# Kernel tuning notes

Measured on AMD Instinct MI355X. Metric: run time of the kernel, lower is better.

The kernel has to match this reference:

```python
import jax, jax.numpy as jnp
import numpy as np

EMBED_DIM = 1024
NUM_HEADS = 16
HEAD_DIM = EMBED_DIM // NUM_HEADS
B, S = 4, 2048


def setup_inputs() -> dict:
    key = jax.random.key(0)
    ks = jax.random.split(key, 9)
    scale = 1.0 / np.sqrt(EMBED_DIM)
    inp = {
        "inputs": jax.random.normal(ks[0], (B, S, EMBED_DIM), dtype=jnp.float32),
        "rotation_params": jax.random.normal(ks[1], (B, S, EMBED_DIM), dtype=jnp.float32),
        "entangle_params": jax.random.normal(ks[2], (B, S, EMBED_DIM), dtype=jnp.float32),
        # Linear weights stored as (out, in) like torch; applied as x @ W.T
        "Wq": jax.random.normal(ks[3], (EMBED_DIM, EMBED_DIM), dtype=jnp.float32) * scale,
        "Wk": jax.random.normal(ks[4], (EMBED_DIM, EMBED_DIM), dtype=jnp.float32) * scale,
        "Wv": jax.random.normal(ks[5], (EMBED_DIM, EMBED_DIM), dtype=jnp.float32) * scale,
        "Wrot": jax.random.normal(ks[6], (EMBED_DIM, EMBED_DIM), dtype=jnp.float32) * scale,
        "Went": jax.random.normal(ks[7], (EMBED_DIM, EMBED_DIM), dtype=jnp.float32) * scale,
        "Wo": jax.random.normal(ks[8], (EMBED_DIM, EMBED_DIM), dtype=jnp.float32) * scale,
    }
    return inp


def _split_heads(x):
    b, s, e = x.shape
    return x.reshape(b, s, NUM_HEADS, HEAD_DIM).transpose(0, 2, 1, 3)  # (B,H,S,D)


def reference(inputs, rotation_params, entangle_params, Wq, Wk, Wv, Wrot, Went, Wo):
    Q = inputs @ Wq.T + rotation_params @ Wrot.T
    K = inputs @ Wk.T + entangle_params @ Went.T
    V = inputs @ Wv.T
    Qh, Kh, Vh = _split_heads(Q), _split_heads(K), _split_heads(V)
    scores = jnp.einsum("bhqd,bhkd->bhqk", Qh, Kh) / jnp.sqrt(jnp.float32(HEAD_DIM))
    attn = jax.nn.softmax(scores, axis=-1)  # dropout p=0 -> identity
    out = jnp.einsum("bhqk,bhkd->bhqd", attn, Vh)
    out = out.transpose(0, 2, 1, 3).reshape(inputs.shape[0], inputs.shape[1], EMBED_DIM)
    return out @ Wo.T
```

## Files before the change

### kernel.cpp

```cpp
#include <hip/hip_runtime.h>
#include <stdint.h>


typedef unsigned short u16;
typedef __bf16 bf16x8 __attribute__((ext_vector_type(8)));
typedef float f32x4 __attribute__((ext_vector_type(4)));
typedef float f32x16 __attribute__((ext_vector_type(16)));
typedef uint32_t u32x4 __attribute__((ext_vector_type(4)));

#define MFMA_BF16(a, b, c) __builtin_amdgcn_mfma_f32_16x16x32_bf16((a), (b), (c), 0, 0, 0)
#define MFMA32(a, b, c)    __builtin_amdgcn_mfma_f32_32x32x16_bf16((a), (b), (c), 0, 0, 0)
#define GAMMA 0.18033688011112042f
#define BHSTRIDE 131072

static __device__ __forceinline__ u16 f2bf(float f) {
    uint32_t u = __builtin_bit_cast(uint32_t, f);
    u = (u + 0x7FFFu + ((u >> 16) & 1u)) >> 16;
    return (u16)u;
}

static __device__ __forceinline__ uint32_t pk_rne2(float a, float b) {
    uint32_t ua = __builtin_bit_cast(uint32_t, a);
    uint32_t ub = __builtin_bit_cast(uint32_t, b);
    ua += 0x7FFFu + ((ua >> 16) & 1u);
    ub += 0x7FFFu + ((ub >> 16) & 1u);
    return __builtin_amdgcn_perm(ub, ua, 0x07060302);
}

static __device__ __forceinline__ void async_copy16(const void* g, void* l) {
    __builtin_amdgcn_global_load_lds((__attribute__((address_space(1))) void*)g,
                                     (__attribute__((address_space(3))) void*)l,
                                     16, 0, 0);
}

static __device__ __forceinline__ uint32_t cvtpk(float a, float b) {
    uint32_t r;
    asm("v_cvt_pk_bf16_f32 %0, %1, %2" : "=v"(r) : "v"(a), "v"(b));
    return r;
}

static __device__ __forceinline__ void plswap(uint32_t& a, uint32_t& b) {
    asm("v_permlane32_swap_b32 %0, %1" : "+v"(a), "+v"(b));
}

static __device__ __forceinline__ bf16x8 mkfrag(uint32_t w0, uint32_t w1,
                                                uint32_t w2, uint32_t w3) {
    u32x4 u = {w0, w1, w2, w3};
    return __builtin_bit_cast(bf16x8, u);
}

struct CvtArgs { const float* s[6]; u16* d[6]; };

__global__ __launch_bounds__(256) void cvt_kernel(CvtArgs a, int nelem) {
    const float* s = a.s[blockIdx.z];
    u16* d = a.d[blockIdx.z];
    int i = (blockIdx.x * 256 + threadIdx.x) * 8;
    float4 f0 = *(const float4*)(s + i);
    float4 f1 = *(const float4*)(s + i + 4);
    uint4 w;
    w.x = pk_rne2(f0.x, f0.y); w.y = pk_rne2(f0.z, f0.w);
    w.z = pk_rne2(f1.x, f1.y); w.w = pk_rne2(f1.z, f1.w);
    *(uint4*)(d + i) = w;
}

template <int AMODE, int CMODE>
__global__ __launch_bounds__(256, 2) void gemm_bt(
    const u16* __restrict__ A0, const u16* __restrict__ W0,
    const u16* __restrict__ A1, const u16* __restrict__ W1,
    void* __restrict__ Cv, int K, int npairs, float scale)
{
    __shared__ __align__(16) u16 lA[128 * 64];
    __shared__ __align__(16) u16 lB[128 * 64];

    const int tid  = threadIdx.x;
    const int lane = tid & 63;
    const int wave = tid >> 6;
    const int wm   = (wave >> 1) * 64;
    const int wn   = (wave & 1) * 64;
    const size_t m0 = (size_t)blockIdx.x * 128;
    const size_t n0 = (size_t)blockIdx.y * 128;

    const int row8 = tid >> 3;
    const int cp   = tid & 7;
    const int fr   = lane & 15;
    const int g    = lane >> 4;

    const size_t bb = (m0 >> 11) * 16;
    const size_t s0 = m0 & 2047;

    f32x4 acc[4][4] = {};

    for (int p = 0; p < npairs; ++p) {
        const u16* A = p ? A1 : A0;
        const u16* W = p ? W1 : W0;
        for (int k0 = 0; k0 < K; k0 += 64) {
            __syncthreads();
#pragma unroll
            for (int it = 0; it < 4; ++it) {
                int row = it * 32 + row8;
                int sc = cp ^ (((row >> 3) ^ row) & 7);
                if (AMODE == 0) {
                    async_copy16(A + ((m0 + row) * (size_t)K + k0 + sc * 8),
                                 (char*)lA + it * 4096 + tid * 16);
                } else {
                    size_t base = (bb + (size_t)(k0 >> 6)) * BHSTRIDE;
                    async_copy16(A + base + (s0 + row) * 64 + sc * 8,
                                 (char*)lA + it * 4096 + tid * 16);
                }
                async_copy16(W + ((n0 + row) * (size_t)K + k0 + sc * 8),
                             (char*)lB + it * 4096 + tid * 16);
            }
            __syncthreads();

            bf16x8 af[4][2], bfm[4][2];
#pragma unroll
            for (int i = 0; i < 4; ++i) {
                int row = wm + i * 16 + fr;
                int sw = ((row >> 3) ^ row) & 7;
                af[i][0] = *(const bf16x8*)(lA + row * 64 + (g ^ sw) * 8);
                af[i][1] = *(const bf16x8*)(lA + row * 64 + ((4 + g) ^ sw) * 8);
            }
#pragma unroll
            for (int j = 0; j < 4; ++j) {
                int row = wn + j * 16 + fr;
                int sw = ((row >> 3) ^ row) & 7;
                bfm[j][0] = *(const bf16x8*)(lB + row * 64 + (g ^ sw) * 8);
                bfm[j][1] = *(const bf16x8*)(lB + row * 64 + ((4 + g) ^ sw) * 8);
            }
#pragma unroll
            for (int i = 0; i < 4; ++i)
#pragma unroll
                for (int j = 0; j < 4; ++j) {
                    acc[i][j] = MFMA_BF16(af[i][0], bfm[j][0], acc[i][j]);
                    acc[i][j] = MFMA_BF16(af[i][1], bfm[j][1], acc[i][j]);
                }
        }
    }

#pragma unroll
    for (int i = 0; i < 4; ++i)
#pragma unroll
        for (int j = 0; j < 4; ++j) {
            if (CMODE == 2) {
                size_t row0 = m0 + wm + i * 16 + g * 4;
                size_t col  = n0 + wn + j * 16 + fr;
                size_t addr = ((row0 >> 11) * 16 + (col >> 6)) * BHSTRIDE
                            + (size_t)(col & 63) * 2048 + (row0 & 2047);
                ushort4 pk;
                pk.x = f2bf(acc[i][j][0] * scale);
                pk.y = f2bf(acc[i][j][1] * scale);
                pk.z = f2bf(acc[i][j][2] * scale);
                pk.w = f2bf(acc[i][j][3] * scale);
                *(ushort4*)((u16*)Cv + addr) = pk;
            } else {
#pragma unroll
                for (int rg = 0; rg < 4; ++rg) {
                    size_t row = m0 + wm + i * 16 + g * 4 + rg;
                    size_t col = n0 + wn + j * 16 + fr;
                    float v = acc[i][j][rg] * scale;
                    if (CMODE == 0) {
                        ((float*)Cv)[row * 1024 + col] = v;
                    } else {
                        size_t addr = ((row >> 11) * 16 + (col >> 6)) * BHSTRIDE
                                    + (row & 2047) * 64 + (col & 63);
                        ((u16*)Cv)[addr] = f2bf(v);
                    }
                }
            }
        }
}

__global__ __launch_bounds__(512, 4) void flash_kernel(
    const u16* __restrict__ Qhm, const u16* __restrict__ Khm,
    const u16* __restrict__ Vt, u16* __restrict__ Ohm)
{
    __shared__ __align__(16) u16 sK[2][128 * 64];
    __shared__ __align__(16) u16 sVt[2][64 * 128];

    const int tid  = threadIdx.x;
    const int lane = tid & 63;
    const int wave = tid >> 6;
    const int l31  = lane & 31;
    const int hg   = lane >> 5;

    const int lin  = blockIdx.x;
    const int slot = lin >> 3;
    const int bh   = (lin & 7) + 8 * (slot >> 3);
    const int q0   = (slot & 7) * 256;

    const u16* Qh = Qhm + (size_t)bh * BHSTRIDE;
    const u16* Kh = Khm + (size_t)bh * BHSTRIDE;
    const u16* Vh = Vt  + (size_t)bh * BHSTRIDE;
    u16*       Oh = Ohm + (size_t)bh * BHSTRIDE;

    bf16x8 qbf[4];
#pragma unroll
    for (int dc = 0; dc < 4; ++dc)
        qbf[dc] = *(const bf16x8*)(Qh +
            (size_t)(q0 + wave * 32 + l31) * 64 + dc * 16 + hg * 8);

    f32x16 oacc[2] = {};
    float lsum = 0.0f;

    const int krow9 = tid >> 3, kcp = tid & 7;
    const int vd5   = tid >> 4, vcp = tid & 15;

    auto stage = [&](int buf, int kt) {
#pragma unroll
        for (int it = 0; it < 2; ++it) {
            int row = it * 64 + krow9;
            int sc = kcp ^ (((row >> 3) ^ row) & 7);
            async_copy16(Kh + (size_t)(kt * 128 + row) * 64 + sc * 8,
                         (char*)(&sK[buf][0]) + it * 8192 + tid * 16);
        }
#pragma unroll
        for (int it = 0; it < 2; ++it) {
            int d = it * 32 + vd5;
            int sc = vcp ^ (d & 15);
            async_copy16(Vh + (size_t)d * 2048 + kt * 128 + sc * 8,
                         (char*)(&sVt[buf][0]) + it * 8192 + tid * 16);
        }
    };

    auto qk = [&](const u16* sKc, int kc) -> f32x16 {
        f32x16 sa = {};
        const int krow = kc * 32 + l31;
        const int ksw = ((krow >> 3) ^ krow) & 7;
#pragma unroll
        for (int dc = 0; dc < 4; ++dc) {
            bf16x8 ka = *(const bf16x8*)(sKc + krow * 64 + ((dc * 2 + hg) ^ ksw) * 8);
            sa = MFMA32(ka, qbf[dc], sa);
        }
        return sa;
    };

    auto sm = [&](const f32x16& sa, bf16x8& o0, bf16x8& o1) {
        float p[16];
#pragma unroll
        for (int r = 0; r < 16; ++r) {
            p[r] = exp2f(sa[r]);
            lsum += p[r];
        }
        uint32_t w0 = cvtpk(p[0],  p[1]),  w1 = cvtpk(p[2],  p[3]);
        uint32_t w2 = cvtpk(p[4],  p[5]),  w3 = cvtpk(p[6],  p[7]);
        uint32_t w4 = cvtpk(p[8],  p[9]),  w5 = cvtpk(p[10], p[11]);
        uint32_t w6 = cvtpk(p[12], p[13]), w7 = cvtpk(p[14], p[15]);
        plswap(w0, w2); plswap(w1, w3);
        plswap(w4, w6); plswap(w5, w7);
        o0 = mkfrag(w0, w1, w2, w3);
        o1 = mkfrag(w4, w5, w6, w7);
    };

    auto pv = [&](const u16* sVc, int kc, bf16x8 pa0, bf16x8 pa1) {
        bf16x8 vb[2][2];
#pragma unroll
        for (int sub = 0; sub < 2; ++sub)
#pragma unroll
            for (int dt = 0; dt < 2; ++dt) {
                int dr = dt * 32 + l31;
                vb[sub][dt] = *(const bf16x8*)(sVc + dr * 128 +
                    ((kc * 4 + sub * 2 + hg) ^ (dr & 15)) * 8);
            }
        oacc[0] = MFMA32(pa0, vb[0][0], oacc[0]);
        oacc[1] = MFMA32(pa0, vb[0][1], oacc[1]);
        oacc[0] = MFMA32(pa1, vb[1][0], oacc[0]);
        oacc[1] = MFMA32(pa1, vb[1][1], oacc[1]);
    };

    stage(0, 0);
    __syncthreads();

    int cur = 0;
    for (int kt = 0; kt < 16; ++kt) {
        const u16* sKc = &sK[cur][0];
        const u16* sVc = &sVt[cur][0];

        f32x16 saA = qk(sKc, 0);
        f32x16 saB = qk(sKc, 1);
        if (kt < 15) stage(cur ^ 1, kt + 1);

        bf16x8 a0, a1, b0, b1;
        sm(saA, a0, a1);  saA = qk(sKc, 2);  pv(sVc, 0, a0, a1);
        sm(saB, b0, b1);  saB = qk(sKc, 3);  pv(sVc, 1, b0, b1);
        sm(saA, a0, a1);                     pv(sVc, 2, a0, a1);
        sm(saB, b0, b1);                     pv(sVc, 3, b0, b1);

        __syncthreads();
        cur ^= 1;
    }

    {
        float l = lsum;
        l += __shfl_xor(l, 32);
        float inv = 1.0f / l;
#pragma unroll
        for (int r = 0; r < 16; ++r) {
            int row = (r & 3) + 4 * hg + 8 * (r >> 2);
            float invr = __shfl(inv, row);
            size_t grow = (size_t)q0 + wave * 32 + row;
            Oh[grow * 64 + l31]      = f2bf(oacc[0][r] * invr);
            Oh[grow * 64 + 32 + l31] = f2bf(oacc[1][r] * invr);
        }
    }
}

extern "C" void kernel_launch(void* const* d_in, const int* in_sizes, int n_in,
                              void* d_out, int out_size, void* d_ws, size_t ws_size,
                              hipStream_t stream)
{
    const float* X    = (const float*)d_in[0];
    const float* R    = (const float*)d_in[1];
    const float* E    = (const float*)d_in[2];
    const float* Wq   = (const float*)d_in[3];
    const float* Wk   = (const float*)d_in[4];
    const float* Wv   = (const float*)d_in[5];
    const float* Wrot = (const float*)d_in[6];
    const float* Went = (const float*)d_in[7];
    const float* Wo   = (const float*)d_in[8];

    const size_t NT = 8192 * 1024;
    const size_t NW = 1024 * 1024;

    u16* Qhm = (u16*)d_out;
    u16* Khm = Qhm + NT;
    u16* Xb  = (u16*)d_ws;
    u16* RVb = Xb + NT;
    u16* EOb = RVb + NT;
    u16* Wqb = EOb + NT;
    u16* Wkb   = Wqb + NW;
    u16* Wvb   = Wkb + NW;
    u16* Wrotb = Wvb + NW;
    u16* Wentb = Wrotb + NW;
    u16* Wob   = Wentb + NW;

    {
        CvtArgs a{};
        a.s[0] = X; a.s[1] = R; a.s[2] = E;
        a.d[0] = Xb; a.d[1] = RVb; a.d[2] = EOb;
        cvt_kernel<<<dim3(4096, 1, 3), 256, 0, stream>>>(a, (int)NT);
    }
    {
        CvtArgs a{};
        a.s[0] = Wq; a.s[1] = Wk; a.s[2] = Wv; a.s[3] = Wrot; a.s[4] = Went; a.s[5] = Wo;
        a.d[0] = Wqb; a.d[1] = Wkb; a.d[2] = Wvb; a.d[3] = Wrotb; a.d[4] = Wentb; a.d[5] = Wob;
        cvt_kernel<<<dim3(512, 1, 6), 256, 0, stream>>>(a, (int)NW);
    }

    dim3 gproj(64, 8);
    gemm_bt<0, 1><<<gproj, 256, 0, stream>>>(Xb, Wqb, RVb, Wrotb, Qhm, 1024, 2, GAMMA);
    gemm_bt<0, 1><<<gproj, 256, 0, stream>>>(Xb, Wkb, EOb, Wentb, Khm, 1024, 2, 1.0f);
    gemm_bt<0, 2><<<gproj, 256, 0, stream>>>(Xb, Wvb, nullptr, nullptr, RVb, 1024, 1, 1.0f);
    flash_kernel<<<dim3(512), 512, 0, stream>>>(Qhm, Khm, RVb, EOb);
    gemm_bt<1, 0><<<gproj, 256, 0, stream>>>(EOb, Wob, nullptr, nullptr, d_out, 1024, 1, 1.0f);
}
```

Measured before the change: 397.2 us.

## Halve flash block to 4 waves, use raw v_exp, split row sums, add sched barriers

The flash attention kernel now launches 1024 blocks of 256 threads, each covering 128 query rows instead of 256, with the K/V staging loops adjusted to match. exp2f is replaced by the raw v_exp_f32 instruction, and the row sum is split across four partial accumulators to shorten the dependency chain. Scheduling barriers are placed between the softmax, QK and PV phases to force the intended interleaving. The smaller blocks mean each K/V tile is loaded from global memory twice as often overall, and the fences stop the compiler from reordering instructions across those phases.

Result: faster. 367.2 us (-7.5%).

```diff
diff --git a/kernel.cpp b/kernel.cpp
--- a/kernel.cpp
+++ b/kernel.cpp
@@ -12,6 +12,7 @@
 #define MFMA32(a, b, c)    __builtin_amdgcn_mfma_f32_32x32x16_bf16((a), (b), (c), 0, 0, 0)
 #define GAMMA 0.18033688011112042f
 #define BHSTRIDE 131072
+#define FENCE() __builtin_amdgcn_sched_barrier(0)
 
 static __device__ __forceinline__ u16 f2bf(float f) {
     uint32_t u = __builtin_bit_cast(uint32_t, f);
@@ -31,6 +32,12 @@
     __builtin_amdgcn_global_load_lds((__attribute__((address_space(1))) void*)g,
                                      (__attribute__((address_space(3))) void*)l,
                                      16, 0, 0);
+}
+
+static __device__ __forceinline__ float aexp2(float x) {
+    float r;
+    asm("v_exp_f32 %0, %1" : "=v"(r) : "v"(x));
+    return r;
 }
 
 static __device__ __forceinline__ uint32_t cvtpk(float a, float b) {
@@ -170,7 +177,7 @@
         }
 }
 
-__global__ __launch_bounds__(512, 4) void flash_kernel(
+__global__ __launch_bounds__(256, 2) void flash_kernel(
     const u16* __restrict__ Qhm, const u16* __restrict__ Khm,
     const u16* __restrict__ Vt, u16* __restrict__ Ohm)
 {
@@ -185,8 +192,8 @@
 
     const int lin  = blockIdx.x;
     const int slot = lin >> 3;
-    const int bh   = (lin & 7) + 8 * (slot >> 3);
-    const int q0   = (slot & 7) * 256;
+    const int bh   = (lin & 7) + 8 * (slot >> 4);
+    const int q0   = (slot & 15) * 128;
 
     const u16* Qh = Qhm + (size_t)bh * BHSTRIDE;
     const u16* Kh = Khm + (size_t)bh * BHSTRIDE;
@@ -200,25 +207,25 @@
             (size_t)(q0 + wave * 32 + l31) * 64 + dc * 16 + hg * 8);
 
     f32x16 oacc[2] = {};
-    float lsum = 0.0f;
-
-    const int krow9 = tid >> 3, kcp = tid & 7;
-    const int vd5   = tid >> 4, vcp = tid & 15;
+    float lsum4[4] = {};
+
+    const int krow8 = tid >> 3, kcp = tid & 7;
+    const int vd16  = tid >> 4, vcp = tid & 15;
 
     auto stage = [&](int buf, int kt) {
 #pragma unroll
-        for (int it = 0; it < 2; ++it) {
-            int row = it * 64 + krow9;
+        for (int it = 0; it < 4; ++it) {
+            int row = it * 32 + krow8;
             int sc = kcp ^ (((row >> 3) ^ row) & 7);
             async_copy16(Kh + (size_t)(kt * 128 + row) * 64 + sc * 8,
-                         (char*)(&sK[buf][0]) + it * 8192 + tid * 16);
-        }
-#pragma unroll
-        for (int it = 0; it < 2; ++it) {
-            int d = it * 32 + vd5;
+                         (char*)(&sK[buf][0]) + it * 4096 + tid * 16);
+        }
+#pragma unroll
+        for (int it = 0; it < 4; ++it) {
+            int d = it * 16 + vd16;
             int sc = vcp ^ (d & 15);
             async_copy16(Vh + (size_t)d * 2048 + kt * 128 + sc * 8,
-                         (char*)(&sVt[buf][0]) + it * 8192 + tid * 16);
+                         (char*)(&sVt[buf][0]) + it * 4096 + tid * 16);
         }
     };
 
@@ -237,10 +244,9 @@
     auto sm = [&](const f32x16& sa, bf16x8& o0, bf16x8& o1) {
         float p[16];
 #pragma unroll
-        for (int r = 0; r < 16; ++r) {
-            p[r] = exp2f(sa[r]);
-            lsum += p[r];
-        }
+        for (int r = 0; r < 16; ++r) p[r] = aexp2(sa[r]);
+#pragma unroll
+        for (int r = 0; r < 16; ++r) lsum4[r & 3] += p[r];
         uint32_t w0 = cvtpk(p[0],  p[1]),  w1 = cvtpk(p[2],  p[3]);
         uint32_t w2 = cvtpk(p[4],  p[5]),  w3 = cvtpk(p[6],  p[7]);
         uint32_t w4 = cvtpk(p[8],  p[9]),  w5 = cvtpk(p[10], p[11]);
@@ -278,19 +284,26 @@
         f32x16 saA = qk(sKc, 0);
         f32x16 saB = qk(sKc, 1);
         if (kt < 15) stage(cur ^ 1, kt + 1);
+        FENCE();
 
         bf16x8 a0, a1, b0, b1;
-        sm(saA, a0, a1);  saA = qk(sKc, 2);  pv(sVc, 0, a0, a1);
-        sm(saB, b0, b1);  saB = qk(sKc, 3);  pv(sVc, 1, b0, b1);
-        sm(saA, a0, a1);                     pv(sVc, 2, a0, a1);
-        sm(saB, b0, b1);                     pv(sVc, 3, b0, b1);
+        sm(saA, a0, a1);   FENCE();
+        saA = qk(sKc, 2);  FENCE();
+        pv(sVc, 0, a0, a1); FENCE();
+        sm(saB, b0, b1);   FENCE();
+        saB = qk(sKc, 3);  FENCE();
+        pv(sVc, 1, b0, b1); FENCE();
+        sm(saA, a0, a1);   FENCE();
+        pv(sVc, 2, a0, a1); FENCE();
+        sm(saB, b0, b1);   FENCE();
+        pv(sVc, 3, b0, b1);
 
         __syncthreads();
         cur ^= 1;
     }
 
     {
-        float l = lsum;
+        float l = (lsum4[0] + lsum4[1]) + (lsum4[2] + lsum4[3]);
         l += __shfl_xor(l, 32);
         float inv = 1.0f / l;
 #pragma unroll
@@ -350,6 +363,6 @@
     gemm_bt<0, 1><<<gproj, 256, 0, stream>>>(Xb, Wqb, RVb, Wrotb, Qhm, 1024, 2, GAMMA);
     gemm_bt<0, 1><<<gproj, 256, 0, stream>>>(Xb, Wkb, EOb, Wentb, Khm, 1024, 2, 1.0f);
     gemm_bt<0, 2><<<gproj, 256, 0, stream>>>(Xb, Wvb, nullptr, nullptr, RVb, 1024, 1, 1.0f);
-    flash_kernel<<<dim3(512), 512, 0, stream>>>(Qhm, Khm, RVb, EOb);
+    flash_kernel<<<dim3(1024), 256, 0, stream>>>(Qhm, Khm, RVb, EOb);
     gemm_bt<1, 0><<<gproj, 256, 0, stream>>>(EOb, Wob, nullptr, nullptr, d_out, 1024, 1, 1.0f);
 }
```
